# Kernel tuning notes

Hardware: AMD Instinct MI355X
Metric: run time of the kernel (lower is better)

Reference implementation:

```python
import jax, jax.numpy as jnp
import numpy as np
from jax.scipy.stats import norm

E = 8          # num experts
R = 16         # LoRA rank
K = 1          # top-k (top-1 gating)
NOISE_EPS = 1e-2


def setup_inputs() -> dict:
    key = jax.random.key(0)
    ks = jax.random.split(key, 6)
    B, T, D = 8, 1024, 1024
    tokens = jax.random.normal(ks[0], (B, T, D), jnp.float32)
    w_gate = jax.random.normal(ks[1], (D, E), jnp.float32) * 0.02
    w_noise = jax.random.normal(ks[2], (D, E), jnp.float32) * 0.02
    lora_a = jax.random.normal(ks[3], (E, R, D), jnp.float32) / np.sqrt(D).astype(np.float32)
    lora_b = jax.random.normal(ks[4], (E, 3 * D, R), jnp.float32) * 0.02
    noise = jax.random.normal(ks[5], (B * T, E), jnp.float32)  # gating noise (randn_like)
    return dict(tokens=tokens, w_gate=w_gate, w_noise=w_noise,
                lora_a=lora_a, lora_b=lora_b, noise=noise)


def reference(tokens, w_gate, w_noise, lora_a, lora_b, noise):
    B, T, D = tokens.shape
    x = tokens.reshape(B * T, D)                       # [N, D]
    N = x.shape[0]

    # --- noisy top-k gating (train mode) ---
    clean_logits = x @ w_gate                          # [N, E]
    noise_stddev = jax.nn.softplus(x @ w_noise) + NOISE_EPS
    logits = clean_logits + noise * noise_stddev       # noisy logits

    m = min(K + 1, E)
    top_vals, top_idx = jax.lax.top_k(logits, m)       # [N, K+1]
    topk_gates = jax.nn.softmax(top_vals[:, :K], axis=1)
    topk_idx = top_idx[:, :K]

    gates = jnp.zeros((N, E), x.dtype).at[jnp.arange(N)[:, None], topk_idx].set(topk_gates)
    importance = gates.sum(0)                          # [E]

    # --- smooth load estimate (prob each token's noisy logit is in top-k) ---
    thr_in = top_vals[:, K][:, None]                   # (K+1)-th value if expert were in
    thr_out = top_vals[:, K - 1][:, None]              # K-th value if expert were out
    is_in = logits > thr_in
    prob = jnp.where(is_in,
                     norm.cdf((clean_logits - thr_in) / noise_stddev),
                     norm.cdf((clean_logits - thr_out) / noise_stddev))
    load = prob.sum(0)                                 # [E]

    # --- dispatch / per-expert LoRA / gated combine ---
    # SparseDispatcher math is equivalent to gate-weighted sum over experts
    # (gates are zero except at the selected experts).
    h = jnp.einsum('nd,erd->ner', x, lora_a)           # [N, E, R] (cheap: R small)
    gh = gates[:, :, None] * h                         # apply gate before up-proj
    out = jnp.einsum('ner,eor->no', gh, lora_b)        # [N, 3D]

    return out.reshape(B, T, 3 * D), importance, load
```

## Files before the change

kernel.cpp:

```cpp
#include <hip/hip_runtime.h>
#include <math.h>

#define N_TOK 8192
#define DIM   1024
#define NE    8
#define NR    16
#define NO    3072
#define OUT_ELEMS (N_TOK * NO)

__device__ __forceinline__ float softplusf(float z) {
  return z > 0.f ? z + log1pf(expf(-z)) : log1pf(expf(z));
}
__device__ __forceinline__ float ncdf(float z) {
  return 0.5f * erfcf(-z * 0.70710678118654752f);
}

#define FMA4(A, S, W) { (A).x = fmaf((S),(W).x,(A).x); (A).y = fmaf((S),(W).y,(A).y); \
                        (A).z = fmaf((S),(W).z,(A).z); (A).w = fmaf((S),(W).w,(A).w); }
#define DOT4ACC(ACC, X, W) ACC = fmaf((X).x,(W).x, fmaf((X).y,(W).y, fmaf((X).z,(W).z, fmaf((X).w,(W).w,(ACC)))))
#define Z4 make_float4(0.f,0.f,0.f,0.f)

__global__ __launch_bounds__(256) void kA9(const float* __restrict__ x,
    const float* __restrict__ wg, const float* __restrict__ wn,
    const float* __restrict__ nz, int* __restrict__ eid, float* __restrict__ part,
    int* __restrict__ fill) {
  __shared__ float xl[16 * 132];
  __shared__ float wl[128 * 20];
  __shared__ float accd[16 * 16 * 20];
  __shared__ float lgS[16 * 20];
  int t = threadIdx.x;
  int n0 = blockIdx.x << 4;
  if (blockIdx.x == 0 && t < 8) fill[t] = 0;
  int tokq = t & 3, og = (t >> 2) & 3, kh = t >> 4;
  int tx = t >> 4, jx = t & 15;
  int kw = t >> 1, hw = t & 1;
  const float* xsrc = x + (size_t)(n0 + tx) * DIM + (jx << 3);
  const float* wsrc = (hw == 0) ? (wg + (size_t)kw * NE) : (wn + (size_t)kw * NE);
  float4 xa0 = *(const float4*)(xsrc);
  float4 xa1 = *(const float4*)(xsrc + 4);
  float4 wa0 = *(const float4*)(wsrc);
  float4 wa1 = *(const float4*)(wsrc + 4);
  float4 acc0 = Z4, acc1 = Z4, acc2 = Z4, acc3 = Z4;
  for (int c = 0; c < 8; ++c) {
    __syncthreads();
    *(float4*)&xl[tx * 132 + (jx << 3)]     = xa0;
    *(float4*)&xl[tx * 132 + (jx << 3) + 4] = xa1;
    *(float4*)&wl[kw * 20 + (hw << 3)]      = wa0;
    *(float4*)&wl[kw * 20 + (hw << 3) + 4]  = wa1;
    __syncthreads();
    if (c < 7) {
      int xo = (c + 1) << 7;
      xa0 = *(const float4*)(xsrc + xo);
      xa1 = *(const float4*)(xsrc + xo + 4);
      int wo = (c + 1) << 10;
      wa0 = *(const float4*)(wsrc + wo);
      wa1 = *(const float4*)(wsrc + wo + 4);
    }
    #pragma unroll
    for (int k4 = 0; k4 < 2; ++k4) {
      int kk = (kh << 3) + (k4 << 2);
      float4 xv0 = *(const float4*)&xl[(tokq +  0) * 132 + kk];
      float4 xv1 = *(const float4*)&xl[(tokq +  4) * 132 + kk];
      float4 xv2 = *(const float4*)&xl[(tokq +  8) * 132 + kk];
      float4 xv3 = *(const float4*)&xl[(tokq + 12) * 132 + kk];
      const float* wb = &wl[kk * 20 + (og << 2)];
      float4 w0 = *(const float4*)(wb + 0);
      float4 w1 = *(const float4*)(wb + 20);
      float4 w2 = *(const float4*)(wb + 40);
      float4 w3 = *(const float4*)(wb + 60);
      FMA4(acc0, xv0.x, w0); FMA4(acc0, xv0.y, w1); FMA4(acc0, xv0.z, w2); FMA4(acc0, xv0.w, w3);
      FMA4(acc1, xv1.x, w0); FMA4(acc1, xv1.y, w1); FMA4(acc1, xv1.z, w2); FMA4(acc1, xv1.w, w3);
      FMA4(acc2, xv2.x, w0); FMA4(acc2, xv2.y, w1); FMA4(acc2, xv2.z, w2); FMA4(acc2, xv2.w, w3);
      FMA4(acc3, xv3.x, w0); FMA4(acc3, xv3.y, w1); FMA4(acc3, xv3.z, w2); FMA4(acc3, xv3.w, w3);
    }
  }
  { int b = kh * 320 + (og << 2);
    *(float4*)&accd[b + (tokq +  0) * 20] = acc0;
    *(float4*)&accd[b + (tokq +  4) * 20] = acc1;
    *(float4*)&accd[b + (tokq +  8) * 20] = acc2;
    *(float4*)&accd[b + (tokq + 12) * 20] = acc3; }
  __syncthreads();
  { int ts = t >> 4, o = t & 15;
    float s = 0.f;
    #pragma unroll
    for (int k2 = 0; k2 < 16; ++k2) s += accd[k2 * 320 + ts * 20 + o];
    lgS[ts * 20 + o] = s; }
  __syncthreads();
  if (t < 16) {
    int n = n0 + t;
    float cl[8], st[8], lg[8];
    float4 nzv0 = *(const float4*)(nz + (size_t)n * NE);
    float4 nzv1 = *(const float4*)(nz + (size_t)n * NE + 4);
    float nzv[8] = {nzv0.x, nzv0.y, nzv0.z, nzv0.w, nzv1.x, nzv1.y, nzv1.z, nzv1.w};
    #pragma unroll
    for (int e = 0; e < 8; ++e) cl[e] = lgS[t * 20 + e];
    #pragma unroll
    for (int e = 0; e < 8; ++e) {
      st[e] = softplusf(lgS[t * 20 + 8 + e]) + 0.01f;
      lg[e] = fmaf(nzv[e], st[e], cl[e]);
    }
    float m1 = -1e30f, m2 = -1e30f; int idx = 0;
    #pragma unroll
    for (int e = 0; e < 8; ++e) {
      float v = lg[e];
      if (v > m1)      { m2 = m1; m1 = v; idx = e; }
      else if (v > m2) { m2 = v; }
    }
    eid[n] = idx;
    float pr[8], cw[8];
    #pragma unroll
    for (int e = 0; e < 8; ++e) {
      float thr = (lg[e] > m2) ? m2 : m1;
      pr[e] = ncdf((cl[e] - thr) / st[e]);
    }
    #pragma unroll
    for (int e = 0; e < 8; ++e) cw[e] = (float)__popcll(__ballot(idx == e));
    #pragma unroll
    for (int e = 0; e < 8; ++e) {
      #pragma unroll
      for (int off = 1; off <= 8; off <<= 1) pr[e] += __shfl_xor(pr[e], off);
    }
    if (t == 0) {
      #pragma unroll
      for (int e = 0; e < 8; ++e) {
        part[blockIdx.x * 16 + e]     = cw[e];
        part[blockIdx.x * 16 + 8 + e] = pr[e];
      }
    }
  }
}

__global__ __launch_bounds__(256) void kC(const float* __restrict__ part,
    const int* __restrict__ eid, int* __restrict__ fill, int* __restrict__ bucket,
    float* __restrict__ outIL, int* __restrict__ counts) {
  __shared__ float red[16][16];
  __shared__ int cnt_s[8], lcnt[8], lbase[8];
  int t = threadIdx.x;
  int s = t & 15, g = t >> 4;
  float sum = 0.f;
  #pragma unroll
  for (int j = 0; j < 32; ++j) sum += part[(g + 16 * j) * 16 + s];
  red[g][s] = sum;
  if (t < 8) lcnt[t] = 0;
  __syncthreads();
  if (t < 16) {
    float tot = 0.f;
    #pragma unroll
    for (int gg = 0; gg < 16; ++gg) tot += red[gg][t];
    if (blockIdx.x == 0) outIL[t] = tot;
    if (t < 8) {
      cnt_s[t] = (int)(tot + 0.5f);
      if (blockIdx.x == 0) counts[t] = (int)(tot + 0.5f);
    }
  }
  __syncthreads();
  int n = blockIdx.x * 256 + t;
  int e = eid[n];
  int rank = atomicAdd(&lcnt[e], 1);
  __syncthreads();
  if (t < 8) lbase[t] = atomicAdd(&fill[t], lcnt[t]);
  __syncthreads();
  int off = 0;
  #pragma unroll
  for (int i = 0; i < 8; ++i) if (i < e) off += cnt_s[i];
  bucket[off + lbase[e] + rank] = n;
}

__global__ __launch_bounds__(256) void kD9b(const float* __restrict__ x,
    const float* __restrict__ la, const int* __restrict__ counts,
    const int* __restrict__ bucket, float* __restrict__ h) {
  __shared__ float xl[16 * 132];
  __shared__ float wl[16 * 132];
  __shared__ float accd[16 * 16 * 20];
  __shared__ float hS[16 * 20];
  __shared__ int toks[16];
  int t = threadIdx.x;
  int tokq = t & 3, rg = (t >> 2) & 3, kh = t >> 4;
  int tx = t >> 4, jx = t & 15;
  for (int tt = 0; tt < 2; ++tt) {
    int tile = (blockIdx.x << 1) + tt;
    int e = -1, jt = 0, off = 0;
    { int tot = 0, o = 0;
      #pragma unroll
      for (int i = 0; i < 8; ++i) {
        int c = counts[i]; int nt = (c + 15) >> 4;
        if (e < 0 && tile < tot + nt) { e = i; jt = tile - tot; off = o; }
        tot += nt; o += c;
      } }
    if (e < 0) continue;
    int cnt = counts[e];
    int p0 = off + (jt << 4);
    int valid = min(16, cnt - (jt << 4));
    if (t < 16) toks[t] = bucket[p0 + min(t, valid - 1)];
    __syncthreads();
    const float* xsrc = x + (size_t)toks[tx] * DIM + (jx << 3);
    const float* wsrc = la + (size_t)e * (NR * DIM) + (size_t)tx * DIM + (jx << 3);
    float4 xa0 = *(const float4*)(xsrc);
    float4 xa1 = *(const float4*)(xsrc + 4);
    float4 wa0 = *(const float4*)(wsrc);
    float4 wa1 = *(const float4*)(wsrc + 4);
    float4 acc0 = Z4, acc1 = Z4, acc2 = Z4, acc3 = Z4;
    for (int c = 0; c < 8; ++c) {
      __syncthreads();
      *(float4*)&xl[tx * 132 + (jx << 3)]     = xa0;
      *(float4*)&xl[tx * 132 + (jx << 3) + 4] = xa1;
      *(float4*)&wl[tx * 132 + (jx << 3)]     = wa0;
      *(float4*)&wl[tx * 132 + (jx << 3) + 4] = wa1;
      __syncthreads();
      if (c < 7) {
        int ko = (c + 1) << 7;
        xa0 = *(const float4*)(xsrc + ko);
        xa1 = *(const float4*)(xsrc + ko + 4);
        wa0 = *(const float4*)(wsrc + ko);
        wa1 = *(const float4*)(wsrc + ko + 4);
      }
      #pragma unroll
      for (int k4 = 0; k4 < 2; ++k4) {
        int kk = (kh << 3) + (k4 << 2);
        float4 xv0 = *(const float4*)&xl[(tokq +  0) * 132 + kk];
        float4 xv1 = *(const float4*)&xl[(tokq +  4) * 132 + kk];
        float4 xv2 = *(const float4*)&xl[(tokq +  8) * 132 + kk];
        float4 xv3 = *(const float4*)&xl[(tokq + 12) * 132 + kk];
        const float* wb = &wl[(rg << 2) * 132 + kk];
        float4 a0 = *(const float4*)(wb + 0);
        float4 a1 = *(const float4*)(wb + 132);
        float4 a2 = *(const float4*)(wb + 264);
        float4 a3 = *(const float4*)(wb + 396);
        DOT4ACC(acc0.x, xv0, a0); DOT4ACC(acc0.y, xv0, a1); DOT4ACC(acc0.z, xv0, a2); DOT4ACC(acc0.w, xv0, a3);
        DOT4ACC(acc1.x, xv1, a0); DOT4ACC(acc1.y, xv1, a1); DOT4ACC(acc1.z, xv1, a2); DOT4ACC(acc1.w, xv1, a3);
        DOT4ACC(acc2.x, xv2, a0); DOT4ACC(acc2.y, xv2, a1); DOT4ACC(acc2.z, xv2, a2); DOT4ACC(acc2.w, xv2, a3);
        DOT4ACC(acc3.x, xv3, a0); DOT4ACC(acc3.y, xv3, a1); DOT4ACC(acc3.z, xv3, a2); DOT4ACC(acc3.w, xv3, a3);
      }
    }
    { int b = kh * 320 + (rg << 2);
      *(float4*)&accd[b + (tokq +  0) * 20] = acc0;
      *(float4*)&accd[b + (tokq +  4) * 20] = acc1;
      *(float4*)&accd[b + (tokq +  8) * 20] = acc2;
      *(float4*)&accd[b + (tokq + 12) * 20] = acc3; }
    __syncthreads();
    { int ts = t >> 4, rr = t & 15;
      float s = 0.f;
      #pragma unroll
      for (int k2 = 0; k2 < 16; ++k2) s += accd[k2 * 320 + ts * 20 + rr];
      hS[ts * 20 + rr] = s; }
    __syncthreads();
    if (t < 64) {
      int tk = t >> 2, rq = (t & 3) << 2;
      if (tk < valid) {
        float4 v = make_float4(hS[tk * 20 + rq + 0], hS[tk * 20 + rq + 1],
                               hS[tk * 20 + rq + 2], hS[tk * 20 + rq + 3]);
        *(float4*)(h + (size_t)(p0 + tk) * NR + rq) = v;
      }
    }
    __syncthreads();
  }
}

__global__ __launch_bounds__(256) void kE(const float* __restrict__ h,
    const float* __restrict__ lb, const int* __restrict__ counts,
    const int* __restrict__ bucket, float* __restrict__ out) {
  __shared__ float bt[16][260];
  __shared__ float ht[16][64];
  __shared__ int toks[64];
  int tile = blockIdx.y;
  int e = -1, jt = 0, off = 0;
  { int tot = 0, o = 0;
    #pragma unroll
    for (int i = 0; i < 8; ++i) {
      int c = counts[i]; int nt = (c + 63) >> 6;
      if (e < 0 && tile < tot + nt) { e = i; jt = tile - tot; off = o; }
      tot += nt; o += c;
    } }
  if (e < 0) return;
  int cnt = counts[e];
  int p0 = off + (jt << 6);
  int valid = min(64, cnt - (jt << 6));
  int o0 = blockIdx.x << 8;
  int t = threadIdx.x;
  if (t < 64) toks[t] = bucket[p0 + min(t, valid - 1)];
  const float* bbase = lb + ((size_t)e * NO + o0) * NR;
  #pragma unroll
  for (int kk = 0; kk < 4; ++kk) {
    int idx = (kk << 8) + t;
    int o = idx >> 2, rq = (idx & 3) << 2;
    float4 v = *(const float4*)(bbase + o * NR + rq);
    bt[rq + 0][o] = v.x; bt[rq + 1][o] = v.y; bt[rq + 2][o] = v.z; bt[rq + 3][o] = v.w;
  }
  { int tok = t >> 2, rq = (t & 3) << 2;
    float4 v = *(const float4*)(h + (size_t)(p0 + min(tok, valid - 1)) * NR + rq);
    ht[rq + 0][tok] = v.x; ht[rq + 1][tok] = v.y; ht[rq + 2][tok] = v.z; ht[rq + 3][tok] = v.w; }
  __syncthreads();
  int og = t & 31, tokg = t >> 5;
  int ob = og << 2, tb = tokg << 3;
  float4 z = Z4;
  float4 aL0=z,aL1=z,aL2=z,aL3=z,aL4=z,aL5=z,aL6=z,aL7=z;
  float4 aH0=z,aH1=z,aH2=z,aH3=z,aH4=z,aH5=z,aH6=z,aH7=z;
  #pragma unroll
  for (int r = 0; r < 16; ++r) {
    float4 blo = *(const float4*)&bt[r][ob];
    float4 bhi = *(const float4*)&bt[r][ob + 128];
    float4 h0  = *(const float4*)&ht[r][tb];
    float4 h1  = *(const float4*)&ht[r][tb + 4];
    FMA4(aL0, h0.x, blo); FMA4(aH0, h0.x, bhi);
    FMA4(aL1, h0.y, blo); FMA4(aH1, h0.y, bhi);
    FMA4(aL2, h0.z, blo); FMA4(aH2, h0.z, bhi);
    FMA4(aL3, h0.w, blo); FMA4(aH3, h0.w, bhi);
    FMA4(aL4, h1.x, blo); FMA4(aH4, h1.x, bhi);
    FMA4(aL5, h1.y, blo); FMA4(aH5, h1.y, bhi);
    FMA4(aL6, h1.z, blo); FMA4(aH6, h1.z, bhi);
    FMA4(aL7, h1.w, blo); FMA4(aH7, h1.w, bhi);
  }
  #define ST(J, AL, AH) { int tt = tb + (J); if (tt < valid) { \
      float* p = out + (size_t)toks[tt] * NO + o0 + ob; \
      *(float4*)p = AL; *(float4*)(p + 128) = AH; } }
  ST(0, aL0, aH0); ST(1, aL1, aH1); ST(2, aL2, aH2); ST(3, aL3, aH3);
  ST(4, aL4, aH4); ST(5, aL5, aH5); ST(6, aL6, aH6); ST(7, aL7, aH7);
  #undef ST
}

extern "C" void kernel_launch(void* const* d_in, const int* in_sizes, int n_in,
                              void* d_out, int out_size, void* d_ws, size_t ws_size,
                              hipStream_t stream) {
  const float* x  = (const float*)d_in[0];
  const float* wg = (const float*)d_in[1];
  const float* wn = (const float*)d_in[2];
  const float* la = (const float*)d_in[3];
  const float* lb = (const float*)d_in[4];
  const float* nz = (const float*)d_in[5];
  float* out = (float*)d_out;

  char* ws = (char*)d_ws;
  float* h        = (float*)(ws);
  int*   eid      = (int*)  (ws + 524288);
  int*   bucket   = (int*)  (ws + 557056);
  float* partials = (float*)(ws + 589824);
  int*   counts   = (int*)  (ws + 622592);
  int*   fill     = (int*)  (ws + 622624);

  kA9<<<512, 256, 0, stream>>>(x, wg, wn, nz, eid, partials, fill);
  kC<<<32, 256, 0, stream>>>(partials, eid, fill, bucket, out + OUT_ELEMS, counts);
  kD9b<<<260, 256, 0, stream>>>(x, la, counts, bucket, h);
  kE<<<dim3(12, 135), 256, 0, stream>>>(h, lb, counts, bucket, out);
}
```

Baseline: 76.19 us.

## Fuse gating, bucketing and LoRA down-projection into one persistent kernel with grid barriers

```diff
diff --git a/kernel.cpp b/kernel.cpp
--- a/kernel.cpp
+++ b/kernel.cpp
@@ -7,6 +7,7 @@
 #define NR    16
 #define NO    3072
 #define OUT_ELEMS (N_TOK * NO)
+#define NBLK  512
 
 __device__ __forceinline__ float softplusf(float z) {
   return z > 0.f ? z + log1pf(expf(-z)) : log1pf(expf(z));
@@ -20,179 +21,189 @@
 #define DOT4ACC(ACC, X, W) ACC = fmaf((X).x,(W).x, fmaf((X).y,(W).y, fmaf((X).z,(W).z, fmaf((X).w,(W).w,(ACC)))))
 #define Z4 make_float4(0.f,0.f,0.f,0.f)
 
-__global__ __launch_bounds__(256) void kA9(const float* __restrict__ x,
+__global__ __launch_bounds__(256, 2) void kF(const float* __restrict__ x,
     const float* __restrict__ wg, const float* __restrict__ wn,
-    const float* __restrict__ nz, int* __restrict__ eid, float* __restrict__ part,
-    int* __restrict__ fill) {
+    const float* __restrict__ nz, const float* __restrict__ la,
+    float* __restrict__ part, int* __restrict__ fill,
+    unsigned int* __restrict__ barcnt, int* __restrict__ bucket,
+    float* __restrict__ outIL, int* __restrict__ counts_g, float* __restrict__ h) {
   __shared__ float xl[16 * 132];
-  __shared__ float wl[128 * 20];
+  __shared__ float wlA[128 * 20];
+  __shared__ float wlC[16 * 132];
   __shared__ float accd[16 * 16 * 20];
   __shared__ float lgS[16 * 20];
+  __shared__ float hS[16 * 20];
+  __shared__ float red[16][16];
+  __shared__ int eid_sh[16], rank_sh[16], cnt_s[8], lcnt[8], lbase[8], toks[16];
   int t = threadIdx.x;
-  int n0 = blockIdx.x << 4;
-  if (blockIdx.x == 0 && t < 8) fill[t] = 0;
-  int tokq = t & 3, og = (t >> 2) & 3, kh = t >> 4;
-  int tx = t >> 4, jx = t & 15;
-  int kw = t >> 1, hw = t & 1;
-  const float* xsrc = x + (size_t)(n0 + tx) * DIM + (jx << 3);
-  const float* wsrc = (hw == 0) ? (wg + (size_t)kw * NE) : (wn + (size_t)kw * NE);
-  float4 xa0 = *(const float4*)(xsrc);
-  float4 xa1 = *(const float4*)(xsrc + 4);
-  float4 wa0 = *(const float4*)(wsrc);
-  float4 wa1 = *(const float4*)(wsrc + 4);
-  float4 acc0 = Z4, acc1 = Z4, acc2 = Z4, acc3 = Z4;
-  for (int c = 0; c < 8; ++c) {
-    __syncthreads();
-    *(float4*)&xl[tx * 132 + (jx << 3)]     = xa0;
-    *(float4*)&xl[tx * 132 + (jx << 3) + 4] = xa1;
-    *(float4*)&wl[kw * 20 + (hw << 3)]      = wa0;
-    *(float4*)&wl[kw * 20 + (hw << 3) + 4]  = wa1;
-    __syncthreads();
-    if (c < 7) {
-      int xo = (c + 1) << 7;
-      xa0 = *(const float4*)(xsrc + xo);
-      xa1 = *(const float4*)(xsrc + xo + 4);
-      int wo = (c + 1) << 10;
-      wa0 = *(const float4*)(wsrc + wo);
-      wa1 = *(const float4*)(wsrc + wo + 4);
-    }
-    #pragma unroll
-    for (int k4 = 0; k4 < 2; ++k4) {
-      int kk = (kh << 3) + (k4 << 2);
-      float4 xv0 = *(const float4*)&xl[(tokq +  0) * 132 + kk];
-      float4 xv1 = *(const float4*)&xl[(tokq +  4) * 132 + kk];
-      float4 xv2 = *(const float4*)&xl[(tokq +  8) * 132 + kk];
-      float4 xv3 = *(const float4*)&xl[(tokq + 12) * 132 + kk];
-      const float* wb = &wl[kk * 20 + (og << 2)];
-      float4 w0 = *(const float4*)(wb + 0);
-      float4 w1 = *(const float4*)(wb + 20);
-      float4 w2 = *(const float4*)(wb + 40);
-      float4 w3 = *(const float4*)(wb + 60);
-      FMA4(acc0, xv0.x, w0); FMA4(acc0, xv0.y, w1); FMA4(acc0, xv0.z, w2); FMA4(acc0, xv0.w, w3);
-      FMA4(acc1, xv1.x, w0); FMA4(acc1, xv1.y, w1); FMA4(acc1, xv1.z, w2); FMA4(acc1, xv1.w, w3);
-      FMA4(acc2, xv2.x, w0); FMA4(acc2, xv2.y, w1); FMA4(acc2, xv2.z, w2); FMA4(acc2, xv2.w, w3);
-      FMA4(acc3, xv3.x, w0); FMA4(acc3, xv3.y, w1); FMA4(acc3, xv3.z, w2); FMA4(acc3, xv3.w, w3);
-    }
-  }
-  { int b = kh * 320 + (og << 2);
-    *(float4*)&accd[b + (tokq +  0) * 20] = acc0;
-    *(float4*)&accd[b + (tokq +  4) * 20] = acc1;
-    *(float4*)&accd[b + (tokq +  8) * 20] = acc2;
-    *(float4*)&accd[b + (tokq + 12) * 20] = acc3; }
-  __syncthreads();
-  { int ts = t >> 4, o = t & 15;
-    float s = 0.f;
-    #pragma unroll
-    for (int k2 = 0; k2 < 16; ++k2) s += accd[k2 * 320 + ts * 20 + o];
-    lgS[ts * 20 + o] = s; }
-  __syncthreads();
-  if (t < 16) {
-    int n = n0 + t;
-    float cl[8], st[8], lg[8];
-    float4 nzv0 = *(const float4*)(nz + (size_t)n * NE);
-    float4 nzv1 = *(const float4*)(nz + (size_t)n * NE + 4);
-    float nzv[8] = {nzv0.x, nzv0.y, nzv0.z, nzv0.w, nzv1.x, nzv1.y, nzv1.z, nzv1.w};
-    #pragma unroll
-    for (int e = 0; e < 8; ++e) cl[e] = lgS[t * 20 + e];
-    #pragma unroll
-    for (int e = 0; e < 8; ++e) {
-      st[e] = softplusf(lgS[t * 20 + 8 + e]) + 0.01f;
-      lg[e] = fmaf(nzv[e], st[e], cl[e]);
-    }
-    float m1 = -1e30f, m2 = -1e30f; int idx = 0;
-    #pragma unroll
-    for (int e = 0; e < 8; ++e) {
-      float v = lg[e];
-      if (v > m1)      { m2 = m1; m1 = v; idx = e; }
-      else if (v > m2) { m2 = v; }
-    }
-    eid[n] = idx;
-    float pr[8], cw[8];
-    #pragma unroll
-    for (int e = 0; e < 8; ++e) {
-      float thr = (lg[e] > m2) ? m2 : m1;
-      pr[e] = ncdf((cl[e] - thr) / st[e]);
-    }
-    #pragma unroll
-    for (int e = 0; e < 8; ++e) cw[e] = (float)__popcll(__ballot(idx == e));
-    #pragma unroll
-    for (int e = 0; e < 8; ++e) {
-      #pragma unroll
-      for (int off = 1; off <= 8; off <<= 1) pr[e] += __shfl_xor(pr[e], off);
-    }
-    if (t == 0) {
+  int bid = blockIdx.x;
+  int n0 = bid << 4;
+  if (bid == 0 && t < 8) fill[t] = 0;
+
+  {
+    int tokq = t & 3, og = (t >> 2) & 3, kh = t >> 4;
+    int tx = t >> 4, jx = t & 15;
+    int kw = t >> 1, hw = t & 1;
+    const float* xsrc = x + (size_t)(n0 + tx) * DIM + (jx << 3);
+    const float* wsrc = (hw == 0) ? (wg + (size_t)kw * NE) : (wn + (size_t)kw * NE);
+    float4 xa0 = *(const float4*)(xsrc);
+    float4 xa1 = *(const float4*)(xsrc + 4);
+    float4 wa0 = *(const float4*)(wsrc);
+    float4 wa1 = *(const float4*)(wsrc + 4);
+    float4 acc0 = Z4, acc1 = Z4, acc2 = Z4, acc3 = Z4;
+    for (int c = 0; c < 8; ++c) {
+      __syncthreads();
+      *(float4*)&xl[tx * 132 + (jx << 3)]      = xa0;
+      *(float4*)&xl[tx * 132 + (jx << 3) + 4]  = xa1;
+      *(float4*)&wlA[kw * 20 + (hw << 3)]      = wa0;
+      *(float4*)&wlA[kw * 20 + (hw << 3) + 4]  = wa1;
+      __syncthreads();
+      if (c < 7) {
+        int xo = (c + 1) << 7;
+        xa0 = *(const float4*)(xsrc + xo);
+        xa1 = *(const float4*)(xsrc + xo + 4);
+        int wo = (c + 1) << 10;
+        wa0 = *(const float4*)(wsrc + wo);
+        wa1 = *(const float4*)(wsrc + wo + 4);
+      }
+      #pragma unroll
+      for (int k4 = 0; k4 < 2; ++k4) {
+        int kk = (kh << 3) + (k4 << 2);
+        float4 xv0 = *(const float4*)&xl[(tokq +  0) * 132 + kk];
+        float4 xv1 = *(const float4*)&xl[(tokq +  4) * 132 + kk];
+        float4 xv2 = *(const float4*)&xl[(tokq +  8) * 132 + kk];
+        float4 xv3 = *(const float4*)&xl[(tokq + 12) * 132 + kk];
+        const float* wb = &wlA[kk * 20 + (og << 2)];
+        float4 w0 = *(const float4*)(wb + 0);
+        float4 w1 = *(const float4*)(wb + 20);
+        float4 w2 = *(const float4*)(wb + 40);
+        float4 w3 = *(const float4*)(wb + 60);
+        FMA4(acc0, xv0.x, w0); FMA4(acc0, xv0.y, w1); FMA4(acc0, xv0.z, w2); FMA4(acc0, xv0.w, w3);
+        FMA4(acc1, xv1.x, w0); FMA4(acc1, xv1.y, w1); FMA4(acc1, xv1.z, w2); FMA4(acc1, xv1.w, w3);
+        FMA4(acc2, xv2.x, w0); FMA4(acc2, xv2.y, w1); FMA4(acc2, xv2.z, w2); FMA4(acc2, xv2.w, w3);
+        FMA4(acc3, xv3.x, w0); FMA4(acc3, xv3.y, w1); FMA4(acc3, xv3.z, w2); FMA4(acc3, xv3.w, w3);
+      }
+    }
+    { int b = kh * 320 + (og << 2);
+      *(float4*)&accd[b + (tokq +  0) * 20] = acc0;
+      *(float4*)&accd[b + (tokq +  4) * 20] = acc1;
+      *(float4*)&accd[b + (tokq +  8) * 20] = acc2;
+      *(float4*)&accd[b + (tokq + 12) * 20] = acc3; }
+    __syncthreads();
+    { int ts = t >> 4, o = t & 15;
+      float s = 0.f;
+      #pragma unroll
+      for (int k2 = 0; k2 < 16; ++k2) s += accd[k2 * 320 + ts * 20 + o];
+      lgS[ts * 20 + o] = s; }
+    __syncthreads();
+    if (t < 16) {
+      int n = n0 + t;
+      float cl[8], st[8], lg[8];
+      float4 nzv0 = *(const float4*)(nz + (size_t)n * NE);
+      float4 nzv1 = *(const float4*)(nz + (size_t)n * NE + 4);
+      float nzv[8] = {nzv0.x, nzv0.y, nzv0.z, nzv0.w, nzv1.x, nzv1.y, nzv1.z, nzv1.w};
+      #pragma unroll
+      for (int e = 0; e < 8; ++e) cl[e] = lgS[t * 20 + e];
       #pragma unroll
       for (int e = 0; e < 8; ++e) {
-        part[blockIdx.x * 16 + e]     = cw[e];
-        part[blockIdx.x * 16 + 8 + e] = pr[e];
-      }
-    }
-  }
-}
-
-__global__ __launch_bounds__(256) void kC(const float* __restrict__ part,
-    const int* __restrict__ eid, int* __restrict__ fill, int* __restrict__ bucket,
-    float* __restrict__ outIL, int* __restrict__ counts) {
-  __shared__ float red[16][16];
-  __shared__ int cnt_s[8], lcnt[8], lbase[8];
-  int t = threadIdx.x;
-  int s = t & 15, g = t >> 4;
-  float sum = 0.f;
-  #pragma unroll
-  for (int j = 0; j < 32; ++j) sum += part[(g + 16 * j) * 16 + s];
-  red[g][s] = sum;
-  if (t < 8) lcnt[t] = 0;
-  __syncthreads();
-  if (t < 16) {
-    float tot = 0.f;
-    #pragma unroll
-    for (int gg = 0; gg < 16; ++gg) tot += red[gg][t];
-    if (blockIdx.x == 0) outIL[t] = tot;
-    if (t < 8) {
-      cnt_s[t] = (int)(tot + 0.5f);
-      if (blockIdx.x == 0) counts[t] = (int)(tot + 0.5f);
-    }
-  }
-  __syncthreads();
-  int n = blockIdx.x * 256 + t;
-  int e = eid[n];
-  int rank = atomicAdd(&lcnt[e], 1);
-  __syncthreads();
-  if (t < 8) lbase[t] = atomicAdd(&fill[t], lcnt[t]);
-  __syncthreads();
-  int off = 0;
-  #pragma unroll
-  for (int i = 0; i < 8; ++i) if (i < e) off += cnt_s[i];
-  bucket[off + lbase[e] + rank] = n;
-}
-
-__global__ __launch_bounds__(256) void kD9b(const float* __restrict__ x,
-    const float* __restrict__ la, const int* __restrict__ counts,
-    const int* __restrict__ bucket, float* __restrict__ h) {
-  __shared__ float xl[16 * 132];
-  __shared__ float wl[16 * 132];
-  __shared__ float accd[16 * 16 * 20];
-  __shared__ float hS[16 * 20];
-  __shared__ int toks[16];
-  int t = threadIdx.x;
-  int tokq = t & 3, rg = (t >> 2) & 3, kh = t >> 4;
-  int tx = t >> 4, jx = t & 15;
-  for (int tt = 0; tt < 2; ++tt) {
-    int tile = (blockIdx.x << 1) + tt;
+        st[e] = softplusf(lgS[t * 20 + 8 + e]) + 0.01f;
+        lg[e] = fmaf(nzv[e], st[e], cl[e]);
+      }
+      float m1 = -1e30f, m2 = -1e30f; int idx = 0;
+      #pragma unroll
+      for (int e = 0; e < 8; ++e) {
+        float v = lg[e];
+        if (v > m1)      { m2 = m1; m1 = v; idx = e; }
+        else if (v > m2) { m2 = v; }
+      }
+      eid_sh[t] = idx;
+      float pr[8], cw[8];
+      #pragma unroll
+      for (int e = 0; e < 8; ++e) {
+        float thr = (lg[e] > m2) ? m2 : m1;
+        pr[e] = ncdf((cl[e] - thr) / st[e]);
+      }
+      #pragma unroll
+      for (int e = 0; e < 8; ++e) cw[e] = (float)__popcll(__ballot(idx == e));
+      #pragma unroll
+      for (int e = 0; e < 8; ++e) {
+        #pragma unroll
+        for (int off = 1; off <= 8; off <<= 1) pr[e] += __shfl_xor(pr[e], off);
+      }
+      if (t == 0) {
+        #pragma unroll
+        for (int e = 0; e < 8; ++e) {
+          part[bid * 16 + e]     = cw[e];
+          part[bid * 16 + 8 + e] = pr[e];
+        }
+      }
+    }
+  }
+  __syncthreads();
+  if (t == 0) {
+    __threadfence();
+    __hip_atomic_fetch_add(barcnt, 1u, __ATOMIC_RELEASE, __HIP_MEMORY_SCOPE_AGENT);
+    while (__hip_atomic_load(barcnt, __ATOMIC_ACQUIRE, __HIP_MEMORY_SCOPE_AGENT) < NBLK)
+      __builtin_amdgcn_s_sleep(4);
+    __threadfence();
+  }
+  __syncthreads();
+  {
+    int s = t & 15, g = t >> 4;
+    float sum = 0.f;
+    for (int j = 0; j < 32; ++j) sum += part[(g + 16 * j) * 16 + s];
+    red[g][s] = sum;
+    if (t < 8) lcnt[t] = 0;
+    __syncthreads();
+    if (t < 16) {
+      float tot = 0.f;
+      #pragma unroll
+      for (int gg = 0; gg < 16; ++gg) tot += red[gg][t];
+      if (bid == 0) outIL[t] = tot;
+      if (t < 8) {
+        cnt_s[t] = (int)(tot + 0.5f);
+        if (bid == 0) counts_g[t] = (int)(tot + 0.5f);
+      }
+    }
+    __syncthreads();
+    if (t < 16) rank_sh[t] = atomicAdd(&lcnt[eid_sh[t]], 1);
+    __syncthreads();
+    if (t < 8) lbase[t] = atomicAdd(&fill[t], lcnt[t]);
+    __syncthreads();
+    if (t < 16) {
+      int e = eid_sh[t];
+      int off = 0;
+      #pragma unroll
+      for (int i = 0; i < 8; ++i) if (i < e) off += cnt_s[i];
+      bucket[off + lbase[e] + rank_sh[t]] = n0 + t;
+    }
+  }
+  __syncthreads();
+  if (t == 0) {
+    __threadfence();
+    __hip_atomic_fetch_add(barcnt, 1u, __ATOMIC_RELEASE, __HIP_MEMORY_SCOPE_AGENT);
+    while (__hip_atomic_load(barcnt, __ATOMIC_ACQUIRE, __HIP_MEMORY_SCOPE_AGENT) < 2u * NBLK)
+      __builtin_amdgcn_s_sleep(4);
+    __threadfence();
+  }
+  __syncthreads();
+  for (int tile = bid; tile < 519; tile += NBLK) {
     int e = -1, jt = 0, off = 0;
     { int tot = 0, o = 0;
       #pragma unroll
       for (int i = 0; i < 8; ++i) {
-        int c = counts[i]; int nt = (c + 15) >> 4;
+        int c = cnt_s[i]; int nt = (c + 15) >> 4;
         if (e < 0 && tile < tot + nt) { e = i; jt = tile - tot; off = o; }
         tot += nt; o += c;
       } }
     if (e < 0) continue;
-    int cnt = counts[e];
+    int cnt = cnt_s[e];
     int p0 = off + (jt << 4);
     int valid = min(16, cnt - (jt << 4));
     if (t < 16) toks[t] = bucket[p0 + min(t, valid - 1)];
     __syncthreads();
+    int tokq = t & 3, rg = (t >> 2) & 3, kh = t >> 4;
+    int tx = t >> 4, jx = t & 15;
     const float* xsrc = x + (size_t)toks[tx] * DIM + (jx << 3);
     const float* wsrc = la + (size_t)e * (NR * DIM) + (size_t)tx * DIM + (jx << 3);
     float4 xa0 = *(const float4*)(xsrc);
@@ -202,10 +213,10 @@
     float4 acc0 = Z4, acc1 = Z4, acc2 = Z4, acc3 = Z4;
     for (int c = 0; c < 8; ++c) {
       __syncthreads();
-      *(float4*)&xl[tx * 132 + (jx << 3)]     = xa0;
-      *(float4*)&xl[tx * 132 + (jx << 3) + 4] = xa1;
-      *(float4*)&wl[tx * 132 + (jx << 3)]     = wa0;
-      *(float4*)&wl[tx * 132 + (jx << 3) + 4] = wa1;
+      *(float4*)&xl[tx * 132 + (jx << 3)]      = xa0;
+      *(float4*)&xl[tx * 132 + (jx << 3) + 4]  = xa1;
+      *(float4*)&wlC[tx * 132 + (jx << 3)]     = wa0;
+      *(float4*)&wlC[tx * 132 + (jx << 3) + 4] = wa1;
       __syncthreads();
       if (c < 7) {
         int ko = (c + 1) << 7;
@@ -221,7 +232,7 @@
         float4 xv1 = *(const float4*)&xl[(tokq +  4) * 132 + kk];
         float4 xv2 = *(const float4*)&xl[(tokq +  8) * 132 + kk];
         float4 xv3 = *(const float4*)&xl[(tokq + 12) * 132 + kk];
-        const float* wb = &wl[(rg << 2) * 132 + kk];
+        const float* wb = &wlC[(rg << 2) * 132 + kk];
         float4 a0 = *(const float4*)(wb + 0);
         float4 a1 = *(const float4*)(wb + 132);
         float4 a2 = *(const float4*)(wb + 264);
@@ -330,15 +341,15 @@
   float* out = (float*)d_out;
 
   char* ws = (char*)d_ws;
-  float* h        = (float*)(ws);
-  int*   eid      = (int*)  (ws + 524288);
-  int*   bucket   = (int*)  (ws + 557056);
-  float* partials = (float*)(ws + 589824);
-  int*   counts   = (int*)  (ws + 622592);
-  int*   fill     = (int*)  (ws + 622624);
-
-  kA9<<<512, 256, 0, stream>>>(x, wg, wn, nz, eid, partials, fill);
-  kC<<<32, 256, 0, stream>>>(partials, eid, fill, bucket, out + OUT_ELEMS, counts);
-  kD9b<<<260, 256, 0, stream>>>(x, la, counts, bucket, h);
+  float*        h        = (float*)(ws);
+  int*          bucket   = (int*)  (ws + 524288);
+  float*        partials = (float*)(ws + 557056);
+  int*          counts   = (int*)  (ws + 589824);
+  int*          fill     = (int*)  (ws + 589856);
+  unsigned int* barcnt   = (unsigned int*)(ws + 589888);
+
+  hipMemsetAsync(barcnt, 0, 4, stream);
+  kF<<<NBLK, 256, 0, stream>>>(x, wg, wn, nz, la, partials, fill, barcnt,
+                               bucket, out + OUT_ELEMS, counts, h);
   kE<<<dim3(12, 135), 256, 0, stream>>>(h, lb, counts, bucket, out);
 }
```

Result: slower. 174.5 us (+129.1%).
